# Kernel optimization log

Hardware: AMD Instinct MI355X
Metric: run time of the kernel (lower is better)

Reference implementation:

```python
import jax, jax.numpy as jnp
import numpy as np

B, T, D, H, L = 8, 150, 30, 5, 3
HD = D // H  # 6
ORIG = (300, 74, 35)


def setup_inputs() -> dict:
    key = jax.random.key(0)
    ks = iter(jax.random.split(key, 40))
    def g(shape, s=0.05):
        return jax.random.normal(next(ks), shape, dtype=jnp.float32) * s
    return {
        "x_l": g((B, T, ORIG[0]), 1.0),
        "x_a": g((B, T, ORIG[1]), 1.0),
        "x_v": g((B, T, ORIG[2]), 1.0),
        "Wl": g((D, ORIG[0])),
        "Wa": g((D, ORIG[1])),
        "Wv": g((D, ORIG[2])),
        "in_w": g((2, L, 3 * D, D)),
        "in_b": jnp.zeros((2, L, 3 * D), jnp.float32),
        "out_w": g((2, L, D, D)),
        "out_b": jnp.zeros((2, L, D), jnp.float32),
        "lin1_w": g((2, L, 4 * D, D)),
        "lin1_b": jnp.zeros((2, L, 4 * D), jnp.float32),
        "lin2_w": g((2, L, D, 4 * D)),
        "lin2_b": jnp.zeros((2, L, D), jnp.float32),
        "n1_g": jnp.ones((2, L, D), jnp.float32),
        "n1_b": jnp.zeros((2, L, D), jnp.float32),
        "n2_g": jnp.ones((2, L, D), jnp.float32),
        "n2_b": jnp.zeros((2, L, D), jnp.float32),
        "p1_w": g((2 * D, 2 * D)),
        "p1_b": jnp.zeros((2 * D,), jnp.float32),
        "p2_w": g((2 * D, 2 * D)),
        "p2_b": jnp.zeros((2 * D,), jnp.float32),
        "ow": g((1, 2 * D)),
        "ob": jnp.zeros((1,), jnp.float32),
    }


def _ln(x, g, b, eps=1e-5):
    m = x.mean(-1, keepdims=True)
    v = jnp.var(x, axis=-1, keepdims=True)  # biased var, matches torch LayerNorm
    return (x - m) * jax.lax.rsqrt(v + eps) * g + b


def _heads(x):  # [Tt, B, D] -> [B*H, Tt, HD]
    Tt = x.shape[0]
    return x.reshape(Tt, B * H, HD).transpose(1, 0, 2)


def _layer(x, xk, xv, p):
    iw, ib, ow, ob, w1, b1, w2, b2, g1, bb1, g2, bb2 = p
    res = x
    xn, kn, vn = _ln(x, g1, bb1), _ln(xk, g1, bb1), _ln(xv, g1, bb1)
    q = (xn @ iw[:D].T + ib[:D]) * (HD ** -0.5)
    k = kn @ iw[D:2 * D].T + ib[D:2 * D]
    v = vn @ iw[2 * D:].T + ib[2 * D:]
    qh, kh, vh = _heads(q), _heads(k), _heads(v)
    # trilinear scores: [B*H, Tq, Tk, Tv]
    aw = jnp.einsum('iat,ibt,ict->iabc', qh, kh, vh)
    fused = aw.mean(-1) + aw.max(-1)          # fuse over value axis -> [B*H, Tq, Tk]
    fused = jax.nn.softmax(fused, axis=-1)
    attn = jnp.einsum('iab,ibt->iat', fused, qh)  # NB: original bmm uses q, not v
    attn = attn.transpose(1, 0, 2).reshape(-1, B, D)
    x = res + (attn @ ow.T + ob)
    res = x
    xn = _ln(x, g2, bb2)
    x = jax.nn.relu(xn @ w1.T + b1) @ w2.T + b2
    return res + x


def reference(x_l, x_a, x_v, Wl, Wa, Wv, in_w, in_b, out_w, out_b,
              lin1_w, lin1_b, lin2_w, lin2_b, n1_g, n1_b, n2_g, n2_b,
              p1_w, p1_b, p2_w, p2_b, ow, ob):
    pl = (x_l @ Wl.T).transpose(1, 0, 2)  # [T, B, D] (conv1d k=1, no bias)
    pa = (x_a @ Wa.T).transpose(1, 0, 2)
    pv = (x_v @ Wv.T).transpose(1, 0, 2)
    hs = []
    for s, (kk, vv) in enumerate(((pa, pv), (pv, pa))):
        h = pl
        for l in range(L):
            p = (in_w[s, l], in_b[s, l], out_w[s, l], out_b[s, l],
                 lin1_w[s, l], lin1_b[s, l], lin2_w[s, l], lin2_b[s, l],
                 n1_g[s, l], n1_b[s, l], n2_g[s, l], n2_b[s, l])
            h = _layer(h, kk, vv, p)
        hs.append(h[-1])  # last timestep [B, D]
    last_hs = jnp.concatenate(hs, axis=1)  # [B, 2D]
    proj = jax.nn.relu(last_hs @ p1_w.T + p1_b) @ p2_w.T + p2_b + last_hs
    out = proj @ ow.T + ob
    return (out, last_hs)
```

## Files before the change

### kernel.cpp

```cpp
#include <hip/hip_runtime.h>
#include <math.h>

#define BB 8
#define TT 150
#define DD 30
#define HH 5
#define HD 6
#define LL 3
#define NI 40
#define ROWF (TT*BB*DD)

typedef _Float16 half8 __attribute__((ext_vector_type(8)));
typedef float f32x16 __attribute__((ext_vector_type(16)));

__device__ __forceinline__ float wsum(float v) {
    #pragma unroll
    for (int m = 32; m > 0; m >>= 1) v += __shfl_xor(v, m, 64);
    return v;
}

__global__ __launch_bounds__(256) void proj_kernel(const float* __restrict__ x,
                                                   const float* __restrict__ W,
                                                   float* __restrict__ out, int Cin) {
    int w = threadIdx.x >> 6, lane = threadIdx.x & 63;
    int unit = blockIdx.x * 4 + w;
    int t = unit / BB, b = unit % BB;
    __shared__ float xr[4][304];
    const float* xp = x + ((size_t)b * TT + t) * Cin;
    for (int j = lane; j < Cin; j += 64) xr[w][j] = xp[j];
    __syncthreads();
    int d = lane >> 1, jh = lane & 1;
    int h1 = Cin >> 1;
    int j0 = jh ? h1 : 0, j1 = jh ? Cin : h1;
    const float* wr = W + (size_t)(d < DD ? d : 0) * Cin;
    float acc = 0.f;
    for (int j = j0; j < j1; j++) acc += xr[w][j] * wr[j];
    acc += __shfl_xor(acc, 1, 64);
    if (jh == 0 && d < DD) out[t * (BB * DD) + b * DD + d] = acc;
}

__global__ __launch_bounds__(256) void lnqkv_kernel(
    const float* __restrict__ h, const float* __restrict__ pl,
    const float* __restrict__ pa, const float* __restrict__ pv,
    const float* __restrict__ in_w, const float* __restrict__ in_b,
    const float* __restrict__ n1g, const float* __restrict__ n1b, int l,
    float* __restrict__ q, float* __restrict__ k, float* __restrict__ v) {
    int w = threadIdx.x >> 6, lane = threadIdx.x & 63;
    int unit = blockIdx.x * 4 + w;
    int s = unit / 1200, tb = unit % 1200;
    int t = tb / BB, b = tb % BB;
    const float* xk = (s == 0) ? pa : pv;
    const float* xv = (s == 0) ? pv : pa;
    int po = s * LL + l;
    const float* iw = in_w + (size_t)po * 90 * 30;
    const float* ib = in_b + (size_t)po * 90;
    const float* g  = n1g + (size_t)po * 30;
    const float* bbv = n1b + (size_t)po * 30;
    __shared__ float xn[4][3][30];
    const float* rows[3];
    rows[0] = (l == 0) ? (pl + (size_t)tb * 30) : (h + (size_t)s * ROWF + (size_t)tb * 30);
    rows[1] = xk + (size_t)tb * 30;
    rows[2] = xv + (size_t)tb * 30;
    for (int r = 0; r < 3; r++) {
        float xval = (lane < 30) ? rows[r][lane] : 0.f;
        float mean = wsum(xval) * (1.f / 30.f);
        float dv = (lane < 30) ? (xval - mean) : 0.f;
        float var = wsum(dv * dv) * (1.f / 30.f);
        float inv = rsqrtf(var + 1e-5f);
        if (lane < 30) xn[w][r][lane] = dv * inv * g[lane] + bbv[lane];
    }
    __syncthreads();
    for (int o = lane; o < 90; o += 64) {
        int which = o / 30, dd = o % 30;
        const float* wr = iw + o * 30;
        const float* xr = xn[w][which];
        float acc = 0.f;
        #pragma unroll 6
        for (int j = 0; j < 30; j++) acc += wr[j] * xr[j];
        acc += ib[o];
        if (which == 0) acc *= 0.40824829046386307f;
        int i = b * HH + dd / HD, hd = dd % HD;
        float* dst = (which == 0) ? q : ((which == 1) ? k : v);
        dst[((size_t)s * NI + i) * (TT * HD) + t * HD + hd] = acc;
    }
}

__global__ __launch_bounds__(256) void score_mfma_kernel(
    const float* __restrict__ q, const float* __restrict__ k, const float* __restrict__ v,
    float* __restrict__ attn) {
    int blk = blockIdx.x;
    int s = blk / 760;
    int rem = blk % 760;
    int i = rem / 19;
    int g = rem % 19;
    int tid = threadIdx.x;
    int wv = tid >> 6, lane = tid & 63;
    int lo = lane & 31, hh = lane >> 5;

    const float* qb = q + ((size_t)s * NI + i) * (TT * HD);
    const float* kb = k + ((size_t)s * NI + i) * (TT * HD);
    const float* vb = v + ((size_t)s * NI + i) * (TT * HD);

    __shared__ float qs[TT * HD];
    __shared__ float ks[TT * HD];
    __shared__ float vs[(TT + 1) * HD];
    for (int idx = tid; idx < TT * HD; idx += 256) {
        qs[idx] = qb[idx];
        ks[idx] = kb[idx];
        vs[idx] = vb[idx];
    }
    __syncthreads();
    if (wv == 0) {
        float v6[6] = {0.f, 0.f, 0.f, 0.f, 0.f, 0.f};
        for (int c = lane; c < TT; c += 64) {
            #pragma unroll
            for (int t = 0; t < 6; t++) v6[t] += vs[c * 6 + t];
        }
        #pragma unroll
        for (int m = 32; m > 0; m >>= 1) {
            #pragma unroll
            for (int t = 0; t < 6; t++) v6[t] += __shfl_xor(v6[t], m, 64);
        }
        if (lane < 6) vs[TT * 6 + lane] = v6[lane] * (1.f / TT);
    }
    __syncthreads();

    half8 bfrag[5], vhalf[5];
    #pragma unroll
    for (int nt = 0; nt < 5; nt++) {
        int rr = nt * 32 + lo;
        half8 bf; half8 vf;
        #pragma unroll
        for (int t = 0; t < 8; t++) { bf[t] = (_Float16)0.f; vf[t] = (_Float16)0.f; }
        if (hh == 0) {
            if (rr < TT) {
                #pragma unroll
                for (int t = 0; t < 6; t++) bf[t] = (_Float16)ks[rr * 6 + t];
            }
            if (rr <= TT) {
                #pragma unroll
                for (int t = 0; t < 6; t++) vf[t] = (_Float16)vs[rr * 6 + t];
            }
        }
        bfrag[nt] = bf; vhalf[nt] = vf;
    }

    f32x16 zacc;
    #pragma unroll
    for (int j = 0; j < 16; j++) zacc[j] = 0.f;

    for (int ap = 0; ap < 2; ap++) {
        int a = g * 8 + wv * 2 + ap;
        if (a >= TT) break;
        half8 qav;
        #pragma unroll
        for (int t = 0; t < 8; t++) qav[t] = (_Float16)((t < 6) ? qs[a * 6 + t] : 0.f);
        half8 afrag[5];
        #pragma unroll
        for (int nt = 0; nt < 5; nt++) afrag[nt] = vhalf[nt] * qav;

        float fsc[5];
        #pragma unroll
        for (int nb = 0; nb < 5; nb++) {
            float rm = -INFINITY;
            #pragma unroll
            for (int ma = 0; ma < 4; ma++) {
                f32x16 acc = __builtin_amdgcn_mfma_f32_32x32x16_f16(afrag[ma], bfrag[nb], zacc, 0, 0, 0);
                float m = fmaxf(acc[0], acc[1]);
                #pragma unroll
                for (int j = 2; j < 16; j += 2) m = fmaxf(fmaxf(m, acc[j]), acc[j + 1]);
                rm = fmaxf(rm, m);
            }
            f32x16 a4 = __builtin_amdgcn_mfma_f32_32x32x16_f16(afrag[4], bfrag[nb], zacc, 0, 0, 0);
            float m4 = fmaxf(a4[0], a4[1]);
            #pragma unroll
            for (int j = 2; j < 10; j += 2) m4 = fmaxf(fmaxf(m4, a4[j]), a4[j + 1]);
            float ext = (hh == 0) ? fmaxf(a4[10], a4[11]) : -INFINITY;
            rm = fmaxf(rm, fmaxf(m4, ext));
            float om = __shfl_xor(a4[10], 32, 64);
            float mn = hh ? a4[10] : om;
            rm = fmaxf(rm, __shfl_xor(rm, 32, 64));
            int b = nb * 32 + lo;
            fsc[nb] = (b < TT) ? (mn + rm) : -INFINITY;
        }
        float m = fsc[0];
        #pragma unroll
        for (int nb = 1; nb < 5; nb++) m = fmaxf(m, fsc[nb]);
        #pragma unroll
        for (int msk = 16; msk > 0; msk >>= 1) m = fmaxf(m, __shfl_xor(m, msk, 64));
        float e[5], es = 0.f;
        #pragma unroll
        for (int nb = 0; nb < 5; nb++) { e[nb] = __expf(fsc[nb] - m); es += e[nb]; }
        #pragma unroll
        for (int msk = 16; msk > 0; msk >>= 1) es += __shfl_xor(es, msk, 64);
        float acc6[6] = {0.f, 0.f, 0.f, 0.f, 0.f, 0.f};
        #pragma unroll
        for (int nb = 0; nb < 5; nb++) {
            int b = nb * 32 + lo;
            int bi = (b < TT) ? b : 0;
            float wgt = e[nb];
            #pragma unroll
            for (int t = 0; t < 6; t++) acc6[t] += wgt * qs[bi * 6 + t];
        }
        #pragma unroll
        for (int msk = 16; msk > 0; msk >>= 1) {
            #pragma unroll
            for (int t = 0; t < 6; t++) acc6[t] += __shfl_xor(acc6[t], msk, 64);
        }
        if (lane == 0) {
            float inv = 1.f / es;
            int bo = i / HH, ho = i % HH;
            float* dst = attn + (size_t)s * ROWF + a * (BB * DD) + bo * DD + ho * HD;
            #pragma unroll
            for (int t = 0; t < 6; t++) dst[t] = acc6[t] * inv;
        }
    }
}

__global__ __launch_bounds__(256) void outffn_kernel(
    const float* __restrict__ attn, const float* __restrict__ pl,
    const float* __restrict__ out_w, const float* __restrict__ out_b,
    const float* __restrict__ l1w, const float* __restrict__ l1b,
    const float* __restrict__ l2w, const float* __restrict__ l2b,
    const float* __restrict__ n2g, const float* __restrict__ n2b, int l,
    float* __restrict__ h) {
    int w = threadIdx.x >> 6, lane = threadIdx.x & 63;
    int unit = blockIdx.x * 4 + w;
    int s = unit / 1200, tb = unit % 1200;
    int po = s * LL + l;
    const float* ow = out_w + (size_t)po * 900;
    const float* ob = out_b + (size_t)po * 30;
    const float* w1 = l1w + (size_t)po * 120 * 30;
    const float* b1 = l1b + (size_t)po * 120;
    const float* w2 = l2w + (size_t)po * 30 * 120;
    const float* b2 = l2b + (size_t)po * 30;
    const float* g  = n2g + (size_t)po * 30;
    const float* bbv = n2b + (size_t)po * 30;
    float* hrow = h + (size_t)s * ROWF + (size_t)tb * 30;
    const float* res = (l == 0) ? (pl + (size_t)tb * 30) : hrow;
    const float* arow = attn + (size_t)s * ROWF + (size_t)tb * 30;
    __shared__ float ar[4][30], x1[4][30], xn[4][30], hid[4][120];
    if (lane < 30) ar[w][lane] = arow[lane];
    __syncthreads();
    float x1v = 0.f;
    if (lane < 30) {
        const float* wr = ow + lane * 30;
        float acc = 0.f;
        #pragma unroll 6
        for (int j = 0; j < 30; j++) acc += wr[j] * ar[w][j];
        x1v = res[lane] + acc + ob[lane];
        x1[w][lane] = x1v;
    }
    float mean = wsum(x1v) * (1.f / 30.f);
    float dv = (lane < 30) ? (x1v - mean) : 0.f;
    float var = wsum(dv * dv) * (1.f / 30.f);
    float inv = rsqrtf(var + 1e-5f);
    if (lane < 30) xn[w][lane] = dv * inv * g[lane] + bbv[lane];
    __syncthreads();
    for (int o = lane; o < 120; o += 64) {
        const float* wr = w1 + o * 30;
        float acc = 0.f;
        #pragma unroll 6
        for (int j = 0; j < 30; j++) acc += wr[j] * xn[w][j];
        hid[w][o] = fmaxf(acc + b1[o], 0.f);
    }
    __syncthreads();
    if (lane < 30) {
        const float* wr = w2 + lane * 120;
        float acc = 0.f;
        #pragma unroll 8
        for (int j = 0; j < 120; j++) acc += wr[j] * hid[w][j];
        hrow[lane] = x1[w][lane] + acc + b2[lane];
    }
}

__global__ __launch_bounds__(256) void head_kernel(
    const float* __restrict__ h,
    const float* __restrict__ p1w, const float* __restrict__ p1b,
    const float* __restrict__ p2w, const float* __restrict__ p2b,
    const float* __restrict__ ow, const float* __restrict__ ob,
    float* __restrict__ out) {
    int tid = threadIdx.x;
    __shared__ float lh[480], hid[480], pr[480];
    for (int idx = tid; idx < 480; idx += 256) {
        int b = idx / 60, j = idx % 60;
        int s = j / 30, d = j % 30;
        float vv = h[(size_t)s * ROWF + 149 * (BB * DD) + b * DD + d];
        lh[idx] = vv;
        out[8 + idx] = vv;
    }
    __syncthreads();
    for (int idx = tid; idx < 480; idx += 256) {
        int b = idx / 60, o = idx % 60;
        const float* wr = p1w + o * 60;
        float acc = p1b[o];
        for (int j = 0; j < 60; j++) acc += wr[j] * lh[b * 60 + j];
        hid[idx] = fmaxf(acc, 0.f);
    }
    __syncthreads();
    for (int idx = tid; idx < 480; idx += 256) {
        int b = idx / 60, d = idx % 60;
        const float* wr = p2w + d * 60;
        float acc = p2b[d];
        for (int j = 0; j < 60; j++) acc += wr[j] * hid[b * 60 + j];
        pr[idx] = acc + lh[idx];
    }
    __syncthreads();
    if (tid < 8) {
        float acc = ob[0];
        for (int j = 0; j < 60; j++) acc += pr[tid * 60 + j] * ow[j];
        out[tid] = acc;
    }
}

extern "C" void kernel_launch(void* const* d_in, const int* in_sizes, int n_in,
                              void* d_out, int out_size, void* d_ws, size_t ws_size,
                              hipStream_t stream) {
    const float* x_l   = (const float*)d_in[0];
    const float* x_a   = (const float*)d_in[1];
    const float* x_v   = (const float*)d_in[2];
    const float* Wl    = (const float*)d_in[3];
    const float* Wa    = (const float*)d_in[4];
    const float* Wv    = (const float*)d_in[5];
    const float* in_w  = (const float*)d_in[6];
    const float* in_b  = (const float*)d_in[7];
    const float* out_w = (const float*)d_in[8];
    const float* out_b = (const float*)d_in[9];
    const float* l1w   = (const float*)d_in[10];
    const float* l1b   = (const float*)d_in[11];
    const float* l2w   = (const float*)d_in[12];
    const float* l2b   = (const float*)d_in[13];
    const float* n1g   = (const float*)d_in[14];
    const float* n1b   = (const float*)d_in[15];
    const float* n2g   = (const float*)d_in[16];
    const float* n2b   = (const float*)d_in[17];
    const float* p1w   = (const float*)d_in[18];
    const float* p1b   = (const float*)d_in[19];
    const float* p2w   = (const float*)d_in[20];
    const float* p2b   = (const float*)d_in[21];
    const float* oww   = (const float*)d_in[22];
    const float* obb   = (const float*)d_in[23];

    float* ws = (float*)d_ws;
    float* pl = ws;
    float* pa = ws + 36000;
    float* pv = ws + 72000;
    float* h  = ws + 108000;
    float* q  = ws + 180000;
    float* kk = ws + 252000;
    float* vv = ws + 324000;
    float* at = ws + 396000;

    proj_kernel<<<300, 256, 0, stream>>>(x_l, Wl, pl, 300);
    proj_kernel<<<300, 256, 0, stream>>>(x_a, Wa, pa, 74);
    proj_kernel<<<300, 256, 0, stream>>>(x_v, Wv, pv, 35);

    for (int l = 0; l < LL; l++) {
        lnqkv_kernel<<<600, 256, 0, stream>>>(h, pl, pa, pv, in_w, in_b, n1g, n1b, l, q, kk, vv);
        score_mfma_kernel<<<1520, 256, 0, stream>>>(q, kk, vv, at);
        outffn_kernel<<<600, 256, 0, stream>>>(at, pl, out_w, out_b, l1w, l1b, l2w, l2b,
                                               n2g, n2b, l, h);
    }
    head_kernel<<<1, 256, 0, stream>>>(h, p1w, p1b, p2w, p2b, oww, obb, (float*)d_out);
}
```

Baseline: 283.2 us.

## Fuse trilinear attention with out-proj/FFN and merge the three input projections

```diff
diff --git a/kernel.cpp b/kernel.cpp
--- a/kernel.cpp
+++ b/kernel.cpp
@@ -9,6 +9,8 @@
 #define LL 3
 #define NI 40
 #define ROWF (TT*BB*DD)
+#define RSTR 8
+#define NR 152
 
 typedef _Float16 half8 __attribute__((ext_vector_type(8)));
 typedef float f32x16 __attribute__((ext_vector_type(16)));
@@ -19,12 +21,18 @@
     return v;
 }
 
-__global__ __launch_bounds__(256) void proj_kernel(const float* __restrict__ x,
-                                                   const float* __restrict__ W,
-                                                   float* __restrict__ out, int Cin) {
+__global__ __launch_bounds__(256) void proj3_kernel(
+    const float* __restrict__ x_l, const float* __restrict__ x_a, const float* __restrict__ x_v,
+    const float* __restrict__ Wl, const float* __restrict__ Wa, const float* __restrict__ Wv,
+    float* __restrict__ pl, float* __restrict__ pa, float* __restrict__ pv) {
     int w = threadIdx.x >> 6, lane = threadIdx.x & 63;
     int unit = blockIdx.x * 4 + w;
-    int t = unit / BB, b = unit % BB;
+    int which = unit / 1200, rowu = unit % 1200;
+    int t = rowu / BB, b = rowu % BB;
+    const float* x = which == 0 ? x_l : (which == 1 ? x_a : x_v);
+    const float* W = which == 0 ? Wl : (which == 1 ? Wa : Wv);
+    float* out = which == 0 ? pl : (which == 1 ? pa : pv);
+    int Cin = which == 0 ? 300 : (which == 1 ? 74 : 35);
     __shared__ float xr[4][304];
     const float* xp = x + ((size_t)b * TT + t) * Cin;
     for (int j = lane; j < Cin; j += 64) xr[w][j] = xp[j];
@@ -85,192 +93,185 @@
     }
 }
 
-__global__ __launch_bounds__(256) void score_mfma_kernel(
+__global__ __launch_bounds__(256) void scoreffn_kernel(
     const float* __restrict__ q, const float* __restrict__ k, const float* __restrict__ v,
-    float* __restrict__ attn) {
-    int blk = blockIdx.x;
-    int s = blk / 760;
-    int rem = blk % 760;
-    int i = rem / 19;
-    int g = rem % 19;
-    int tid = threadIdx.x;
-    int wv = tid >> 6, lane = tid & 63;
-    int lo = lane & 31, hh = lane >> 5;
-
-    const float* qb = q + ((size_t)s * NI + i) * (TT * HD);
-    const float* kb = k + ((size_t)s * NI + i) * (TT * HD);
-    const float* vb = v + ((size_t)s * NI + i) * (TT * HD);
-
-    __shared__ float qs[TT * HD];
-    __shared__ float ks[TT * HD];
-    __shared__ float vs[(TT + 1) * HD];
-    for (int idx = tid; idx < TT * HD; idx += 256) {
-        qs[idx] = qb[idx];
-        ks[idx] = kb[idx];
-        vs[idx] = vb[idx];
-    }
-    __syncthreads();
-    if (wv == 0) {
-        float v6[6] = {0.f, 0.f, 0.f, 0.f, 0.f, 0.f};
-        for (int c = lane; c < TT; c += 64) {
-            #pragma unroll
-            for (int t = 0; t < 6; t++) v6[t] += vs[c * 6 + t];
-        }
-        #pragma unroll
-        for (int m = 32; m > 0; m >>= 1) {
-            #pragma unroll
-            for (int t = 0; t < 6; t++) v6[t] += __shfl_xor(v6[t], m, 64);
-        }
-        if (lane < 6) vs[TT * 6 + lane] = v6[lane] * (1.f / TT);
-    }
-    __syncthreads();
-
-    half8 bfrag[5], vhalf[5];
-    #pragma unroll
-    for (int nt = 0; nt < 5; nt++) {
-        int rr = nt * 32 + lo;
-        half8 bf; half8 vf;
-        #pragma unroll
-        for (int t = 0; t < 8; t++) { bf[t] = (_Float16)0.f; vf[t] = (_Float16)0.f; }
-        if (hh == 0) {
-            if (rr < TT) {
-                #pragma unroll
-                for (int t = 0; t < 6; t++) bf[t] = (_Float16)ks[rr * 6 + t];
-            }
-            if (rr <= TT) {
-                #pragma unroll
-                for (int t = 0; t < 6; t++) vf[t] = (_Float16)vs[rr * 6 + t];
-            }
-        }
-        bfrag[nt] = bf; vhalf[nt] = vf;
-    }
-
-    f32x16 zacc;
-    #pragma unroll
-    for (int j = 0; j < 16; j++) zacc[j] = 0.f;
-
-    for (int ap = 0; ap < 2; ap++) {
-        int a = g * 8 + wv * 2 + ap;
-        if (a >= TT) break;
-        half8 qav;
-        #pragma unroll
-        for (int t = 0; t < 8; t++) qav[t] = (_Float16)((t < 6) ? qs[a * 6 + t] : 0.f);
-        half8 afrag[5];
-        #pragma unroll
-        for (int nt = 0; nt < 5; nt++) afrag[nt] = vhalf[nt] * qav;
-
-        float fsc[5];
-        #pragma unroll
-        for (int nb = 0; nb < 5; nb++) {
-            float rm = -INFINITY;
-            #pragma unroll
-            for (int ma = 0; ma < 4; ma++) {
-                f32x16 acc = __builtin_amdgcn_mfma_f32_32x32x16_f16(afrag[ma], bfrag[nb], zacc, 0, 0, 0);
-                float m = fmaxf(acc[0], acc[1]);
-                #pragma unroll
-                for (int j = 2; j < 16; j += 2) m = fmaxf(fmaxf(m, acc[j]), acc[j + 1]);
-                rm = fmaxf(rm, m);
-            }
-            f32x16 a4 = __builtin_amdgcn_mfma_f32_32x32x16_f16(afrag[4], bfrag[nb], zacc, 0, 0, 0);
-            float m4 = fmaxf(a4[0], a4[1]);
-            #pragma unroll
-            for (int j = 2; j < 10; j += 2) m4 = fmaxf(fmaxf(m4, a4[j]), a4[j + 1]);
-            float ext = (hh == 0) ? fmaxf(a4[10], a4[11]) : -INFINITY;
-            rm = fmaxf(rm, fmaxf(m4, ext));
-            float om = __shfl_xor(a4[10], 32, 64);
-            float mn = hh ? a4[10] : om;
-            rm = fmaxf(rm, __shfl_xor(rm, 32, 64));
-            int b = nb * 32 + lo;
-            fsc[nb] = (b < TT) ? (mn + rm) : -INFINITY;
-        }
-        float m = fsc[0];
-        #pragma unroll
-        for (int nb = 1; nb < 5; nb++) m = fmaxf(m, fsc[nb]);
-        #pragma unroll
-        for (int msk = 16; msk > 0; msk >>= 1) m = fmaxf(m, __shfl_xor(m, msk, 64));
-        float e[5], es = 0.f;
-        #pragma unroll
-        for (int nb = 0; nb < 5; nb++) { e[nb] = __expf(fsc[nb] - m); es += e[nb]; }
-        #pragma unroll
-        for (int msk = 16; msk > 0; msk >>= 1) es += __shfl_xor(es, msk, 64);
-        float acc6[6] = {0.f, 0.f, 0.f, 0.f, 0.f, 0.f};
-        #pragma unroll
-        for (int nb = 0; nb < 5; nb++) {
-            int b = nb * 32 + lo;
-            int bi = (b < TT) ? b : 0;
-            float wgt = e[nb];
-            #pragma unroll
-            for (int t = 0; t < 6; t++) acc6[t] += wgt * qs[bi * 6 + t];
-        }
-        #pragma unroll
-        for (int msk = 16; msk > 0; msk >>= 1) {
-            #pragma unroll
-            for (int t = 0; t < 6; t++) acc6[t] += __shfl_xor(acc6[t], msk, 64);
-        }
-        if (lane == 0) {
-            float inv = 1.f / es;
-            int bo = i / HH, ho = i % HH;
-            float* dst = attn + (size_t)s * ROWF + a * (BB * DD) + bo * DD + ho * HD;
-            #pragma unroll
-            for (int t = 0; t < 6; t++) dst[t] = acc6[t] * inv;
-        }
-    }
-}
-
-__global__ __launch_bounds__(256) void outffn_kernel(
-    const float* __restrict__ attn, const float* __restrict__ pl,
+    const float* __restrict__ pl,
     const float* __restrict__ out_w, const float* __restrict__ out_b,
     const float* __restrict__ l1w, const float* __restrict__ l1b,
     const float* __restrict__ l2w, const float* __restrict__ l2b,
     const float* __restrict__ n2g, const float* __restrict__ n2b, int l,
     float* __restrict__ h) {
-    int w = threadIdx.x >> 6, lane = threadIdx.x & 63;
-    int unit = blockIdx.x * 4 + w;
-    int s = unit / 1200, tb = unit % 1200;
-    int po = s * LL + l;
-    const float* ow = out_w + (size_t)po * 900;
-    const float* ob = out_b + (size_t)po * 30;
-    const float* w1 = l1w + (size_t)po * 120 * 30;
-    const float* b1 = l1b + (size_t)po * 120;
-    const float* w2 = l2w + (size_t)po * 30 * 120;
-    const float* b2 = l2b + (size_t)po * 30;
-    const float* g  = n2g + (size_t)po * 30;
-    const float* bbv = n2b + (size_t)po * 30;
-    float* hrow = h + (size_t)s * ROWF + (size_t)tb * 30;
-    const float* res = (l == 0) ? (pl + (size_t)tb * 30) : hrow;
-    const float* arow = attn + (size_t)s * ROWF + (size_t)tb * 30;
-    __shared__ float ar[4][30], x1[4][30], xn[4][30], hid[4][120];
-    if (lane < 30) ar[w][lane] = arow[lane];
-    __syncthreads();
-    float x1v = 0.f;
-    if (lane < 30) {
-        const float* wr = ow + lane * 30;
-        float acc = 0.f;
-        #pragma unroll 6
-        for (int j = 0; j < 30; j++) acc += wr[j] * ar[w][j];
-        x1v = res[lane] + acc + ob[lane];
-        x1[w][lane] = x1v;
-    }
-    float mean = wsum(x1v) * (1.f / 30.f);
-    float dv = (lane < 30) ? (x1v - mean) : 0.f;
-    float var = wsum(dv * dv) * (1.f / 30.f);
-    float inv = rsqrtf(var + 1e-5f);
-    if (lane < 30) xn[w][lane] = dv * inv * g[lane] + bbv[lane];
-    __syncthreads();
-    for (int o = lane; o < 120; o += 64) {
-        const float* wr = w1 + o * 30;
-        float acc = 0.f;
-        #pragma unroll 6
-        for (int j = 0; j < 30; j++) acc += wr[j] * xn[w][j];
-        hid[w][o] = fmaxf(acc + b1[o], 0.f);
-    }
-    __syncthreads();
-    if (lane < 30) {
-        const float* wr = w2 + lane * 120;
-        float acc = 0.f;
-        #pragma unroll 8
-        for (int j = 0; j < 120; j++) acc += wr[j] * hid[w][j];
-        hrow[lane] = x1[w][lane] + acc + b2[lane];
+    int blk = blockIdx.x;
+    int s = blk / 304;
+    int rem = blk % 304;
+    int b = rem / 38;
+    int g = rem % 38;
+    int tid = threadIdx.x;
+    int wv = tid >> 6, lane = tid & 63;
+    int lo = lane & 31, hf = lane >> 5;
+
+    __shared__ __align__(16) _Float16 qsh[HH][NR * RSTR];
+    __shared__ __align__(16) _Float16 ksh[HH][NR * RSTR];
+    __shared__ __align__(16) _Float16 vsh[HH][NR * RSTR];
+    __shared__ float attnS[4][32];
+    __shared__ float xnS[4][32];
+    __shared__ float hidS[4][128];
+
+    int* qz = (int*)&qsh[0][0];
+    int* kz = (int*)&ksh[0][0];
+    int* vz = (int*)&vsh[0][0];
+    for (int idx = tid; idx < HH * NR * RSTR / 2; idx += 256) {
+        qz[idx] = 0; kz[idx] = 0; vz[idx] = 0;
+    }
+    __syncthreads();
+    const float* qg = q + (size_t)(s * NI + b * HH) * (TT * HD);
+    const float* kg = k + (size_t)(s * NI + b * HH) * (TT * HD);
+    const float* vg = v + (size_t)(s * NI + b * HH) * (TT * HD);
+    for (int idx = tid; idx < HH * TT * HD; idx += 256) {
+        int h5 = idx / (TT * HD);
+        int rr = (idx % (TT * HD)) / HD;
+        int t = idx % HD;
+        int dst = rr * RSTR + t;
+        qsh[h5][dst] = (_Float16)qg[idx];
+        ksh[h5][dst] = (_Float16)kg[idx];
+        vsh[h5][dst] = (_Float16)vg[idx];
+    }
+    __syncthreads();
+    for (int h5 = wv; h5 < HH; h5 += 4) {
+        float v6[6] = {0.f, 0.f, 0.f, 0.f, 0.f, 0.f};
+        for (int c = lane; c < TT; c += 64) {
+            #pragma unroll
+            for (int t = 0; t < 6; t++) v6[t] += (float)vsh[h5][c * RSTR + t];
+        }
+        #pragma unroll
+        for (int m = 32; m > 0; m >>= 1) {
+            #pragma unroll
+            for (int t = 0; t < 6; t++) v6[t] += __shfl_xor(v6[t], m, 64);
+        }
+        if (lane < 6) vsh[h5][TT * RSTR + lane] = (_Float16)(v6[lane] * (1.f / TT));
+    }
+    __syncthreads();
+
+    int a = g * 4 + wv;
+    bool alive = (a < TT);
+
+    f32x16 zacc;
+    #pragma unroll
+    for (int j = 0; j < 16; j++) zacc[j] = 0.f;
+    half8 zero8;
+    #pragma unroll
+    for (int t = 0; t < 8; t++) zero8[t] = (_Float16)0.f;
+
+    if (alive) {
+        for (int h5 = 0; h5 < HH; h5++) {
+            const _Float16* kbase = qsh[0];
+            (void)kbase;
+            half8 qav = *(const half8*)&qsh[h5][a * RSTR];
+            half8 bfrag[5], afrag[5];
+            #pragma unroll
+            for (int nt = 0; nt < 5; nt++) {
+                int rr = nt * 32 + lo;
+                int rc = rr < 151 ? rr : 151;
+                half8 kf = *(const half8*)&ksh[h5][rc * RSTR];
+                half8 vf = *(const half8*)&vsh[h5][rc * RSTR];
+                bfrag[nt] = hf ? zero8 : kf;
+                afrag[nt] = hf ? zero8 : (vf * qav);
+            }
+            float fsc[5];
+            #pragma unroll
+            for (int nb = 0; nb < 5; nb++) {
+                float rm = -INFINITY;
+                #pragma unroll
+                for (int ma = 0; ma < 4; ma++) {
+                    f32x16 acc = __builtin_amdgcn_mfma_f32_32x32x16_f16(afrag[ma], bfrag[nb], zacc, 0, 0, 0);
+                    float m = fmaxf(acc[0], acc[1]);
+                    #pragma unroll
+                    for (int j = 2; j < 16; j += 2) m = fmaxf(fmaxf(m, acc[j]), acc[j + 1]);
+                    rm = fmaxf(rm, m);
+                }
+                f32x16 a4 = __builtin_amdgcn_mfma_f32_32x32x16_f16(afrag[4], bfrag[nb], zacc, 0, 0, 0);
+                float m4 = fmaxf(a4[0], a4[1]);
+                #pragma unroll
+                for (int j = 2; j < 10; j += 2) m4 = fmaxf(fmaxf(m4, a4[j]), a4[j + 1]);
+                float ext = (hf == 0) ? fmaxf(a4[10], a4[11]) : -INFINITY;
+                rm = fmaxf(rm, fmaxf(m4, ext));
+                float om = __shfl_xor(a4[10], 32, 64);
+                float mn = hf ? a4[10] : om;
+                rm = fmaxf(rm, __shfl_xor(rm, 32, 64));
+                int bcol = nb * 32 + lo;
+                fsc[nb] = (bcol < TT) ? (mn + rm) : -INFINITY;
+            }
+            float m = fsc[0];
+            #pragma unroll
+            for (int nb = 1; nb < 5; nb++) m = fmaxf(m, fsc[nb]);
+            #pragma unroll
+            for (int msk = 16; msk > 0; msk >>= 1) m = fmaxf(m, __shfl_xor(m, msk, 64));
+            float e[5], es = 0.f;
+            #pragma unroll
+            for (int nb = 0; nb < 5; nb++) { e[nb] = __expf(fsc[nb] - m); es += e[nb]; }
+            #pragma unroll
+            for (int msk = 16; msk > 0; msk >>= 1) es += __shfl_xor(es, msk, 64);
+            float acc6[6] = {0.f, 0.f, 0.f, 0.f, 0.f, 0.f};
+            #pragma unroll
+            for (int nb = 0; nb < 5; nb++) {
+                int bcol = nb * 32 + lo;
+                int bi = (bcol < TT) ? bcol : 0;
+                float wgt = e[nb];
+                half8 qrow = *(const half8*)&qsh[h5][bi * RSTR];
+                #pragma unroll
+                for (int t = 0; t < 6; t++) acc6[t] += wgt * (float)qrow[t];
+            }
+            #pragma unroll
+            for (int msk = 16; msk > 0; msk >>= 1) {
+                #pragma unroll
+                for (int t = 0; t < 6; t++) acc6[t] += __shfl_xor(acc6[t], msk, 64);
+            }
+            if (lane == 0) {
+                float inv = 1.f / es;
+                #pragma unroll
+                for (int t = 0; t < 6; t++) attnS[wv][h5 * 6 + t] = acc6[t] * inv;
+            }
+        }
+
+        int tb = a * BB + b;
+        int po = s * LL + l;
+        const float* ow = out_w + (size_t)po * 900;
+        const float* ob = out_b + (size_t)po * 30;
+        const float* w1 = l1w + (size_t)po * 120 * 30;
+        const float* b1 = l1b + (size_t)po * 120;
+        const float* w2 = l2w + (size_t)po * 30 * 120;
+        const float* b2 = l2b + (size_t)po * 30;
+        const float* gg = n2g + (size_t)po * 30;
+        const float* bbv = n2b + (size_t)po * 30;
+        float* hrow = h + (size_t)s * ROWF + (size_t)tb * 30;
+        const float* res = (l == 0) ? (pl + (size_t)tb * 30) : hrow;
+        float x1v = 0.f;
+        if (lane < 30) {
+            const float* wr = ow + lane * 30;
+            float acc = 0.f;
+            #pragma unroll 6
+            for (int j = 0; j < 30; j++) acc += wr[j] * attnS[wv][j];
+            x1v = res[lane] + acc + ob[lane];
+        }
+        float mean = wsum(x1v) * (1.f / 30.f);
+        float dv = (lane < 30) ? (x1v - mean) : 0.f;
+        float var = wsum(dv * dv) * (1.f / 30.f);
+        float inv = rsqrtf(var + 1e-5f);
+        if (lane < 30) xnS[wv][lane] = dv * inv * gg[lane] + bbv[lane];
+        for (int o = lane; o < 120; o += 64) {
+            const float* wr = w1 + o * 30;
+            float acc = 0.f;
+            #pragma unroll 6
+            for (int j = 0; j < 30; j++) acc += wr[j] * xnS[wv][j];
+            hidS[wv][o] = fmaxf(acc + b1[o], 0.f);
+        }
+        if (lane < 30) {
+            const float* wr = w2 + lane * 120;
+            float acc = 0.f;
+            #pragma unroll 8
+            for (int j = 0; j < 120; j++) acc += wr[j] * hidS[wv][j];
+            hrow[lane] = x1v + acc + b2[lane];
+        }
     }
 }
 
@@ -349,17 +350,13 @@
     float* q  = ws + 180000;
     float* kk = ws + 252000;
     float* vv = ws + 324000;
-    float* at = ws + 396000;
-
-    proj_kernel<<<300, 256, 0, stream>>>(x_l, Wl, pl, 300);
-    proj_kernel<<<300, 256, 0, stream>>>(x_a, Wa, pa, 74);
-    proj_kernel<<<300, 256, 0, stream>>>(x_v, Wv, pv, 35);
+
+    proj3_kernel<<<900, 256, 0, stream>>>(x_l, x_a, x_v, Wl, Wa, Wv, pl, pa, pv);
 
     for (int l = 0; l < LL; l++) {
         lnqkv_kernel<<<600, 256, 0, stream>>>(h, pl, pa, pv, in_w, in_b, n1g, n1b, l, q, kk, vv);
-        score_mfma_kernel<<<1520, 256, 0, stream>>>(q, kk, vv, at);
-        outffn_kernel<<<600, 256, 0, stream>>>(at, pl, out_w, out_b, l1w, l1b, l2w, l2b,
-                                               n2g, n2b, l, h);
+        scoreffn_kernel<<<608, 256, 0, stream>>>(q, kk, vv, pl, out_w, out_b,
+                                                 l1w, l1b, l2w, l2b, n2g, n2b, l, h);
     }
     head_kernel<<<1, 256, 0, stream>>>(h, p1w, p1b, p2w, p2b, oww, obb, (float*)d_out);
 }
```

Measured after the change: 280.4 us. About the same (-1.0%).
